# Kernel tuning notes

Measured on AMD Instinct MI355X. Metric: run time of the kernel, lower is better.

Reference implementation:

```python
import jax, jax.numpy as jnp
import numpy as np

C = 256
CQK = C // 8  # 32


def setup_inputs() -> dict:
    key = jax.random.key(0)
    ks = jax.random.split(key, 7)
    x = jax.random.normal(ks[0], (4, C, 64, 64), dtype=jnp.float32)
    s = 1.0 / np.sqrt(C)
    Wq = jax.random.normal(ks[1], (CQK, C), dtype=jnp.float32) * s
    bq = jnp.zeros((CQK,), dtype=jnp.float32)
    Wk = jax.random.normal(ks[2], (CQK, C), dtype=jnp.float32) * s
    bk = jnp.zeros((CQK,), dtype=jnp.float32)
    Wv = jax.random.normal(ks[3], (C, C), dtype=jnp.float32) * s
    bv = jnp.zeros((C,), dtype=jnp.float32)
    return {"x": x, "Wq": Wq, "bq": bq, "Wk": Wk, "bk": bk, "Wv": Wv, "bv": bv}


def reference(x, Wq, bq, Wk, bk, Wv, bv):
    B, Cc, H, W = x.shape
    xf = x.reshape(B, Cc, H * W)  # [B, C, HW]
    # 1x1 convs == per-pixel linear projections over channels
    q = jnp.einsum('oc,bcn->bno', Wq, xf) + bq          # [B, HW, C//8]
    k = jnp.einsum('oc,bcn->bon', Wk, xf) + bk[:, None]  # [B, C//8, HW]
    v = jnp.einsum('oc,bcn->bno', Wv, xf) + bv          # [B, HW, C]
    attn = jax.nn.softmax(jnp.einsum('bnd,bdm->bnm', q, k), axis=-1)  # [B, HW, HW]
    out = jnp.einsum('bnm,bmc->bnc', attn, v)           # [B, HW, C]
    return out.transpose(0, 2, 1).reshape(B, Cc, H, W)
```

## Files before the change

### kernel.cpp

```cpp
#include <hip/hip_runtime.h>
#include <hip/hip_bf16.h>


#define N_PIX 4096
#define DQK   32
#define CCH   256
#define LOG2E 1.44269504088896f

typedef __attribute__((ext_vector_type(8))) _Float16 f16x8;
typedef __attribute__((ext_vector_type(4))) _Float16 f16x4;
typedef __attribute__((ext_vector_type(2))) _Float16 f16x2;
typedef __attribute__((ext_vector_type(8))) short    bf16x8;
typedef __attribute__((ext_vector_type(4))) short    bf16x4;
typedef __attribute__((ext_vector_type(4))) float    f32x4;

__device__ inline void barrier_lds() {
    asm volatile("" ::: "memory");
    __builtin_amdgcn_s_waitcnt(0xc07f);
    __builtin_amdgcn_s_barrier();
    asm volatile("" ::: "memory");
}

__device__ inline short bf16bits(float f) {
    __hip_bfloat16 h = __float2bfloat16(f);
    return *(short*)&h;
}

__device__ inline unsigned cvt_pk_bf16(float lo, float hi) {
    unsigned r;
    asm("v_cvt_pk_bf16_f32 %0, %1, %2" : "=v"(r) : "v"(lo), "v"(hi));
    return r;
}

__global__ __launch_bounds__(256) void wpack_kernel(
    const float* __restrict__ Wq, const float* __restrict__ Wk,
    const float* __restrict__ Wv, _Float16* __restrict__ Wp)
{
    const int tid   = threadIdx.x;
    const int wflat = blockIdx.x * 4 + (tid >> 6);
    const int lane  = tid & 63;
    const int L15   = lane & 15;
    const int quad  = lane >> 4;
    const int mt    = wflat >> 3;
    const int ks    = wflat & 7;
    const int m0    = mt * 16;

    const float* Wsrc; int row; float scale = 1.f;
    if (m0 < 32)      { Wsrc = Wq; row = m0 + L15;      scale = LOG2E; }
    else if (m0 < 64) { Wsrc = Wk; row = m0 - 32 + L15; }
    else              { Wsrc = Wv; row = m0 - 64 + L15; }

    const float* p = Wsrc + (size_t)row * 256 + ks * 32 + quad * 8;
    f16x8 h;
    #pragma unroll
    for (int j = 0; j < 8; ++j) h[j] = (_Float16)(p[j] * scale);
    *(f16x8*)(Wp + ((size_t)wflat * 64 + lane) * 8) = h;
}

__global__ __launch_bounds__(512, 4) void qkv_kernel(
    const float* __restrict__ x, const _Float16* __restrict__ Wp,
    const float* __restrict__ bq, const float* __restrict__ bk,
    const float* __restrict__ bv,
    _Float16* __restrict__ qo, _Float16* __restrict__ ko,
    __hip_bfloat16* __restrict__ vp)
{
    __shared__ alignas(16) unsigned char shraw[256 * 40 * 2];
    _Float16       (*xT)[264] = (_Float16 (*)[264])shraw;
    __hip_bfloat16 (*vst)[40] = (__hip_bfloat16 (*)[40])shraw;

    const int idx = blockIdx.x;
    const int b   = (idx & 7) >> 1;
    const int n0  = (((idx >> 3) << 1) | (idx & 1)) * 32;
    const int tid = threadIdx.x;

    {
        const float* xb = x + (size_t)b * CCH * N_PIX;
        float4 ld[2][2];
        int c2s[2], n4s[2];
        #pragma unroll
        for (int pass = 0; pass < 2; ++pass) {
            const int flat = pass * 512 + tid;
            c2s[pass] = (flat >> 3) * 2;
            n4s[pass] = (flat & 7) * 4;
            ld[pass][0] = *(const float4*)(xb + (size_t)c2s[pass]       * N_PIX + n0 + n4s[pass]);
            ld[pass][1] = *(const float4*)(xb + (size_t)(c2s[pass] + 1) * N_PIX + n0 + n4s[pass]);
        }
        #pragma unroll
        for (int pass = 0; pass < 2; ++pass) {
            const float a[4] = {ld[pass][0].x, ld[pass][0].y, ld[pass][0].z, ld[pass][0].w};
            const float c[4] = {ld[pass][1].x, ld[pass][1].y, ld[pass][1].z, ld[pass][1].w};
            #pragma unroll
            for (int i = 0; i < 4; ++i)
                *(f16x2*)(&xT[n4s[pass] + i][c2s[pass]]) =
                    (f16x2){(_Float16)a[i], (_Float16)c[i]};
        }
    }
    __syncthreads();

    const int lane = tid & 63;
    const int wid  = tid >> 6;
    const int L15  = lane & 15;
    const int quad = lane >> 4;
    const int nf   = wid & 1;
    const int mtg  = wid >> 1;

    const f32x4 fz = {0.f, 0.f, 0.f, 0.f};
    f32x4 acc[5];
    #pragma unroll
    for (int mt = 0; mt < 5; ++mt) acc[mt] = fz;

    const _Float16* wpw = Wp + ((size_t)(mtg * 5) * 8 * 64 + lane) * 8;

    #pragma unroll
    for (int ks = 0; ks < 8; ++ks) {
        const f16x8 bfr = *(const f16x8*)(&xT[nf * 16 + L15][ks * 32 + quad * 8]);
        #pragma unroll
        for (int mt = 0; mt < 5; ++mt) {
            const f16x8 afr = *(const f16x8*)(wpw + (size_t)(mt * 8 + ks) * 512);
            acc[mt] = __builtin_amdgcn_mfma_f32_16x16x32_f16(afr, bfr, acc[mt], 0, 0, 0);
        }
    }

    const int np = nf * 16 + L15;
    const int n  = n0 + np;
    #pragma unroll
    for (int mt = 0; mt < 5; ++mt) {
        const int m0 = (mtg * 5 + mt) * 16;
        const f32x4 a = acc[mt];
        if (m0 < 32) {
            const int mr = m0 + quad * 4;
            f16x4 h;
            #pragma unroll
            for (int r = 0; r < 4; ++r) h[r] = (_Float16)(a[r] + bq[mr + r] * LOG2E);
            *(f16x4*)(qo + ((size_t)b * N_PIX + n) * DQK + mr) = h;
        } else if (m0 < 64) {
            const int mr = m0 - 32 + quad * 4;
            f16x4 h;
            #pragma unroll
            for (int r = 0; r < 4; ++r) h[r] = (_Float16)(a[r] + bk[mr + r]);
            *(f16x4*)(ko + ((size_t)b * N_PIX + n) * DQK + mr) = h;
        }
    }

    __syncthreads();

    #pragma unroll
    for (int mt = 0; mt < 5; ++mt) {
        const int m0 = (mtg * 5 + mt) * 16;
        if (m0 >= 64) {
            const int c = m0 - 64 + quad * 4;
            #pragma unroll
            for (int r = 0; r < 4; ++r)
                vst[c + r][np] = __float2bfloat16(acc[mt][r] + bv[c + r]);
        }
    }
    __syncthreads();

    {
        __hip_bfloat16* vpb = vp + (size_t)b * 2048 * 512 + (size_t)((n0 >> 5) * 16) * 512;
        #pragma unroll
        for (int s = 0; s < 2; ++s) {
            const int slot = s * 512 + tid;
            const int cg16 = slot >> 6;
            const int ln   = slot & 63;
            const int qd   = ln >> 4;
            const int l15  = ln & 15;
            const bf16x8 val = *(const bf16x8*)(&vst[cg16 * 16 + l15][qd * 8]);
            *(bf16x8*)(vpb + ((size_t)cg16 * 64 + ln) * 8) = val;
        }
    }
}


#define ATTN_BODY(J, KR, VR, PSRD, DO_S)                                          \
  {                                                                               \
    const bool dos_ = (DO_S);                                                     \
    f32x4 s_ = fz;                                                                \
    if (dos_) s_ = __builtin_amdgcn_mfma_f32_16x16x32_f16(KR, aq, fz, 0, 0, 0);   \
                        \
    {                                                                             \
      const _Float16* kt_ = kb + (size_t)(((J) + 3) & 63) * (64 * DQK);           \
      KR = *(const f16x8*)(kt_ + koff);                                           \
    }                                                                             \
                                                          \
    _Pragma("unroll")                                                             \
    for (int qq_ = 0; qq_ < 2; ++qq_) {                                           \
      _Pragma("unroll")                                                           \
      for (int kk_ = 0; kk_ < 2; ++kk_) {                                         \
        const bf16x8 ap_ = *(const bf16x8*)(                                      \
            &Ps[PSRD][qq_ * 16 + L15][(kk_ * 32 + quad * 8) ^ sw8]);              \
        oacc[qq_][0] = __builtin_amdgcn_mfma_f32_16x16x32_bf16(                   \
            ap_, VR[kk_][0], oacc[qq_][0], 0, 0, 0);                              \
        oacc[qq_][1] = __builtin_amdgcn_mfma_f32_16x16x32_bf16(                   \
            ap_, VR[kk_][1], oacc[qq_][1], 0, 0, 0);                              \
      }                                                                           \
    }                                                                             \
                                                     \
    {                                                                             \
      const __hip_bfloat16* vt_ = vb + (size_t)(((J) + 2) & 63) * (2 * 16 * 512); \
      _Pragma("unroll")                                                           \
      for (int kk_ = 0; kk_ < 2; ++kk_)                                           \
        _Pragma("unroll")                                                         \
        for (int cf_ = 0; cf_ < 2; ++cf_)                                         \
          VR[kk_][cf_] = *(const bf16x8*)(vt_ + voff0 + kk_ * 8192 + cf_ * 512);  \
    }                                                                             \
                                          \
    if (dos_) {                                                                   \
      const float p0_ = exp2f(s_[0]), p1_ = exp2f(s_[1]);                         \
      const float p2_ = exp2f(s_[2]), p3_ = exp2f(s_[3]);                         \
      psum += (p0_ + p1_) + (p2_ + p3_);                                          \
      uint2 pk_;                                                                  \
      pk_.x = cvt_pk_bf16(p0_, p1_);                                              \
      pk_.y = cvt_pk_bf16(p2_, p3_);                                              \
      *(uint2*)(&Ps[(PSRD) ^ 1][qt * 16 + L15][(kt * 16 + quad * 4) ^ sw8]) = pk_;\
    }                                                                             \
    barrier_lds();                                                                \
  }

__global__ __launch_bounds__(512, 4) void attn_kernel(
    const _Float16* __restrict__ qg,
    const _Float16* __restrict__ kg,
    const __hip_bfloat16* __restrict__ vp,
    float* __restrict__ out)
{
    __shared__ alignas(16) __hip_bfloat16 Ps[2][32][72];
    __shared__ float lsum[2][4][16];

    const int idx  = blockIdx.x;
    const int b    = (idx & 7) >> 1;
    const int n0   = (((idx >> 3) << 1) | (idx & 1)) * 32;
    const int tid  = threadIdx.x;
    const int wid  = tid >> 6;
    const int lane = tid & 63;
    const int L15  = lane & 15;
    const int quad = lane >> 4;
    const int qt   = wid & 1;
    const int kt   = wid >> 1;
    const int cg   = wid;
    const int c0   = cg * 32;
    const int sw8  = ((L15 >> 3) & 1) << 3;

    const f32x4 fz = {0.f, 0.f, 0.f, 0.f};

    const f16x8 aq = *(const f16x8*)(qg + ((size_t)b * N_PIX + n0 + qt * 16 + L15) * DQK + quad * 8);

    f32x4 oacc[2][2];
    #pragma unroll
    for (int qq = 0; qq < 2; ++qq)
        #pragma unroll
        for (int cf = 0; cf < 2; ++cf) oacc[qq][cf] = fz;
    float psum = 0.f;

    const _Float16* kb = kg + (size_t)b * N_PIX * DQK;
    const int koff  = (kt * 16 + L15) * DQK + quad * 8;
    const __hip_bfloat16* vb = vp + (size_t)b * 2048 * 512;
    const int voff0 = lane * 8 + cg * 2 * 512;

    f16x8 kA = *(const f16x8*)(kb + (size_t)1 * 64 * DQK + koff);
    f16x8 kB = *(const f16x8*)(kb + (size_t)2 * 64 * DQK + koff);
    bf16x8 vA[2][2], vB[2][2];
    #pragma unroll
    for (int kk = 0; kk < 2; ++kk)
        #pragma unroll
        for (int cf = 0; cf < 2; ++cf) {
            vA[kk][cf] = *(const bf16x8*)(vb +                 voff0 + kk * 8192 + cf * 512);
            vB[kk][cf] = *(const bf16x8*)(vb + (size_t)16384 + voff0 + kk * 8192 + cf * 512);
        }
    {
        const f16x8 k0f = *(const f16x8*)(kb + koff);
        const f32x4 s = __builtin_amdgcn_mfma_f32_16x16x32_f16(k0f, aq, fz, 0, 0, 0);
        const float p0 = exp2f(s[0]), p1 = exp2f(s[1]);
        const float p2 = exp2f(s[2]), p3 = exp2f(s[3]);
        psum += (p0 + p1) + (p2 + p3);
        uint2 pk;
        pk.x = cvt_pk_bf16(p0, p1);
        pk.y = cvt_pk_bf16(p2, p3);
        *(uint2*)(&Ps[0][qt * 16 + L15][(kt * 16 + quad * 4) ^ sw8]) = pk;
    }
    barrier_lds();

    for (int it = 0; it < 64; it += 2) {
        ATTN_BODY(it,     kA, vA, 0, true);
        ATTN_BODY(it + 1, kB, vB, 1, it < 62);
    }

    psum += __shfl_xor(psum, 16, 64);
    psum += __shfl_xor(psum, 32, 64);
    if (quad == 0) lsum[qt][kt][L15] = psum;
    __syncthreads();

    float* ob = out + (size_t)b * CCH * N_PIX;
    #pragma unroll
    for (int qq = 0; qq < 2; ++qq) {
        float inv_l[4];
        #pragma unroll
        for (int r = 0; r < 4; ++r) {
            const int q = quad * 4 + r;
            inv_l[r] = 1.f / (lsum[qq][0][q] + lsum[qq][1][q] +
                              lsum[qq][2][q] + lsum[qq][3][q]);
        }
        #pragma unroll
        for (int cf = 0; cf < 2; ++cf) {
            const int c = c0 + cf * 16 + L15;
            f32x4 o;
            #pragma unroll
            for (int r = 0; r < 4; ++r) o[r] = oacc[qq][cf][r] * inv_l[r];
            *(f32x4*)(ob + (size_t)c * N_PIX + n0 + qq * 16 + quad * 4) = o;
        }
    }
}

extern "C" void kernel_launch(void* const* d_in, const int* in_sizes, int n_in,
                              void* d_out, int out_size, void* d_ws, size_t ws_size,
                              hipStream_t stream) {
    (void)in_sizes; (void)n_in; (void)out_size; (void)ws_size;
    const float* x  = (const float*)d_in[0];
    const float* Wq = (const float*)d_in[1];
    const float* bq = (const float*)d_in[2];
    const float* Wk = (const float*)d_in[3];
    const float* bk = (const float*)d_in[4];
    const float* Wv = (const float*)d_in[5];
    const float* bv = (const float*)d_in[6];

    _Float16* qb = (_Float16*)d_ws;
    _Float16* kb = qb + (size_t)4 * N_PIX * DQK;
    __hip_bfloat16* vpk = (__hip_bfloat16*)(kb + (size_t)4 * N_PIX * DQK);
    _Float16* wp = (_Float16*)(vpk + (size_t)4 * 2048 * 512);
    float* outp = (float*)d_out;

    wpack_kernel<<<40, 256, 0, stream>>>(Wq, Wk, Wv, wp);
    qkv_kernel<<<512, 512, 0, stream>>>(x, wp, bq, bk, bv, qb, kb, vpk);
    attn_kernel<<<512, 512, 0, stream>>>(qb, kb, vpk, outp);
}
```

Before: 147.8 us.

## Warp-specialize attention into separate score and PV wavefronts with 64-query tiles

Restructures the attention kernel into 1024-thread blocks where 8 wavefronts compute QK scores, exp2 and bf16 P tiles, while 8 other wavefronts consume P from LDS and do the PV MFMAs. Each block now covers 64 queries instead of 32, halving the number of blocks and doubling reuse of each V tile loaded. The P tile in LDS is relaid out as pre-packed MFMA fragments to avoid the swizzle. The two roles hand off through double-buffered LDS with a barrier per step. The design relies on score and PV work overlapping across waves, at the cost of a larger block, fewer blocks (256) and idle lanes in whichever role is lighter.

```diff
diff --git a/kernel.cpp b/kernel.cpp
--- a/kernel.cpp
+++ b/kernel.cpp
@@ -19,11 +19,6 @@
     __builtin_amdgcn_s_waitcnt(0xc07f);
     __builtin_amdgcn_s_barrier();
     asm volatile("" ::: "memory");
-}
-
-__device__ inline short bf16bits(float f) {
-    __hip_bfloat16 h = __float2bfloat16(f);
-    return *(short*)&h;
 }
 
 __device__ inline unsigned cvt_pk_bf16(float lo, float hi) {
@@ -172,140 +167,157 @@
 }
 
 
-#define ATTN_BODY(J, KR, VR, PSRD, DO_S)                                          \
+#define PV_BODY(J, VR)                                                            \
   {                                                                               \
-    const bool dos_ = (DO_S);                                                     \
-    f32x4 s_ = fz;                                                                \
-    if (dos_) s_ = __builtin_amdgcn_mfma_f32_16x16x32_f16(KR, aq, fz, 0, 0, 0);   \
-                        \
-    {                                                                             \
-      const _Float16* kt_ = kb + (size_t)(((J) + 3) & 63) * (64 * DQK);           \
-      KR = *(const f16x8*)(kt_ + koff);                                           \
-    }                                                                             \
-                                                          \
+    const int buf_ = (J) & 1;                                                     \
     _Pragma("unroll")                                                             \
-    for (int qq_ = 0; qq_ < 2; ++qq_) {                                           \
+    for (int qq_ = 0; qq_ < 4; ++qq_) {                                           \
       _Pragma("unroll")                                                           \
       for (int kk_ = 0; kk_ < 2; ++kk_) {                                         \
-        const bf16x8 ap_ = *(const bf16x8*)(                                      \
-            &Ps[PSRD][qq_ * 16 + L15][(kk_ * 32 + quad * 8) ^ sw8]);              \
+        const bf16x8 ap_ = *(const bf16x8*)(&Ps[buf_][qq_ * 2 + kk_][quad][L15][0]); \
         oacc[qq_][0] = __builtin_amdgcn_mfma_f32_16x16x32_bf16(                   \
             ap_, VR[kk_][0], oacc[qq_][0], 0, 0, 0);                              \
         oacc[qq_][1] = __builtin_amdgcn_mfma_f32_16x16x32_bf16(                   \
             ap_, VR[kk_][1], oacc[qq_][1], 0, 0, 0);                              \
       }                                                                           \
     }                                                                             \
-                                                     \
-    {                                                                             \
-      const __hip_bfloat16* vt_ = vb + (size_t)(((J) + 2) & 63) * (2 * 16 * 512); \
+    const __hip_bfloat16* vt_ = vb + (size_t)(((J) + 2) & 63) * 16384;            \
+    _Pragma("unroll")                                                             \
+    for (int kk_ = 0; kk_ < 2; ++kk_)                                             \
       _Pragma("unroll")                                                           \
-      for (int kk_ = 0; kk_ < 2; ++kk_)                                           \
-        _Pragma("unroll")                                                         \
-        for (int cf_ = 0; cf_ < 2; ++cf_)                                         \
-          VR[kk_][cf_] = *(const bf16x8*)(vt_ + voff0 + kk_ * 8192 + cf_ * 512);  \
+      for (int cf_ = 0; cf_ < 2; ++cf_)                                           \
+        VR[kk_][cf_] = *(const bf16x8*)(vt_ + voff0 + kk_ * 8192 + cf_ * 512);    \
+  }
+
+#define S_BODY(J, KR0, KR1, DO_S)                                                 \
+  {                                                                               \
+    if (DO_S) {                                                                   \
+      const int bufw_ = ((J) & 1) ^ 1;                                            \
+      const f32x4 s0_ = __builtin_amdgcn_mfma_f32_16x16x32_f16(KR0, aq, fz, 0, 0, 0); \
+      const f32x4 s1_ = __builtin_amdgcn_mfma_f32_16x16x32_f16(KR1, aq, fz, 0, 0, 0); \
+      const _Float16* kp_ = kbp + (size_t)(((J) + 3) & 63) * (64 * DQK);          \
+      KR0 = *(const f16x8*)(kp_ + koff0);                                         \
+      KR1 = *(const f16x8*)(kp_ + koff1);                                         \
+      const float a0_ = exp2f(s0_[0]), a1_ = exp2f(s0_[1]);                       \
+      const float a2_ = exp2f(s0_[2]), a3_ = exp2f(s0_[3]);                       \
+      psum0 += (a0_ + a1_) + (a2_ + a3_);                                         \
+      uint2 w0_; w0_.x = cvt_pk_bf16(a0_, a1_); w0_.y = cvt_pk_bf16(a2_, a3_);    \
+      *(uint2*)(&Ps[bufw_][grp][quad >> 1][L15][(quad & 1) * 4]) = w0_;           \
+      const float b0_ = exp2f(s1_[0]), b1_ = exp2f(s1_[1]);                       \
+      const float b2_ = exp2f(s1_[2]), b3_ = exp2f(s1_[3]);                       \
+      psum1 += (b0_ + b1_) + (b2_ + b3_);                                         \
+      uint2 w1_; w1_.x = cvt_pk_bf16(b0_, b1_); w1_.y = cvt_pk_bf16(b2_, b3_);    \
+      *(uint2*)(&Ps[bufw_][grp][2 + (quad >> 1)][L15][(quad & 1) * 4]) = w1_;     \
     }                                                                             \
-                                          \
-    if (dos_) {                                                                   \
-      const float p0_ = exp2f(s_[0]), p1_ = exp2f(s_[1]);                         \
-      const float p2_ = exp2f(s_[2]), p3_ = exp2f(s_[3]);                         \
-      psum += (p0_ + p1_) + (p2_ + p3_);                                          \
-      uint2 pk_;                                                                  \
-      pk_.x = cvt_pk_bf16(p0_, p1_);                                              \
-      pk_.y = cvt_pk_bf16(p2_, p3_);                                              \
-      *(uint2*)(&Ps[(PSRD) ^ 1][qt * 16 + L15][(kt * 16 + quad * 4) ^ sw8]) = pk_;\
-    }                                                                             \
-    barrier_lds();                                                                \
   }
 
-__global__ __launch_bounds__(512, 4) void attn_kernel(
+__global__ __launch_bounds__(1024, 4) void attn_kernel(
     const _Float16* __restrict__ qg,
     const _Float16* __restrict__ kg,
     const __hip_bfloat16* __restrict__ vp,
     float* __restrict__ out)
 {
-    __shared__ alignas(16) __hip_bfloat16 Ps[2][32][72];
-    __shared__ float lsum[2][4][16];
+    __shared__ __hip_bfloat16 Ps[2][8][4][16][8];
+    __shared__ float lsum[4][4][16];
 
     const int idx  = blockIdx.x;
     const int b    = (idx & 7) >> 1;
-    const int n0   = (((idx >> 3) << 1) | (idx & 1)) * 32;
+    const int n0   = (((idx >> 3) << 1) | (idx & 1)) * 64;
     const int tid  = threadIdx.x;
     const int wid  = tid >> 6;
     const int lane = tid & 63;
     const int L15  = lane & 15;
     const int quad = lane >> 4;
-    const int qt   = wid & 1;
-    const int kt   = wid >> 1;
-    const int cg   = wid;
-    const int c0   = cg * 32;
-    const int sw8  = ((L15 >> 3) & 1) << 3;
+    const bool is_pv = (wid < 8);
 
     const f32x4 fz = {0.f, 0.f, 0.f, 0.f};
 
-    const f16x8 aq = *(const f16x8*)(qg + ((size_t)b * N_PIX + n0 + qt * 16 + L15) * DQK + quad * 8);
-
-    f32x4 oacc[2][2];
-    #pragma unroll
-    for (int qq = 0; qq < 2; ++qq)
-        #pragma unroll
-        for (int cf = 0; cf < 2; ++cf) oacc[qq][cf] = fz;
-    float psum = 0.f;
-
-    const _Float16* kb = kg + (size_t)b * N_PIX * DQK;
-    const int koff  = (kt * 16 + L15) * DQK + quad * 8;
+    const int cg = wid & 7;
     const __hip_bfloat16* vb = vp + (size_t)b * 2048 * 512;
     const int voff0 = lane * 8 + cg * 2 * 512;
-
-    f16x8 kA = *(const f16x8*)(kb + (size_t)1 * 64 * DQK + koff);
-    f16x8 kB = *(const f16x8*)(kb + (size_t)2 * 64 * DQK + koff);
+    f32x4 oacc[4][2];
+    #pragma unroll
+    for (int qq = 0; qq < 4; ++qq) { oacc[qq][0] = fz; oacc[qq][1] = fz; }
     bf16x8 vA[2][2], vB[2][2];
-    #pragma unroll
-    for (int kk = 0; kk < 2; ++kk)
-        #pragma unroll
-        for (int cf = 0; cf < 2; ++cf) {
-            vA[kk][cf] = *(const bf16x8*)(vb +                 voff0 + kk * 8192 + cf * 512);
-            vB[kk][cf] = *(const bf16x8*)(vb + (size_t)16384 + voff0 + kk * 8192 + cf * 512);
-        }
-    {
-        const f16x8 k0f = *(const f16x8*)(kb + koff);
-        const f32x4 s = __builtin_amdgcn_mfma_f32_16x16x32_f16(k0f, aq, fz, 0, 0, 0);
-        const float p0 = exp2f(s[0]), p1 = exp2f(s[1]);
-        const float p2 = exp2f(s[2]), p3 = exp2f(s[3]);
-        psum += (p0 + p1) + (p2 + p3);
-        uint2 pk;
-        pk.x = cvt_pk_bf16(p0, p1);
-        pk.y = cvt_pk_bf16(p2, p3);
-        *(uint2*)(&Ps[0][qt * 16 + L15][(kt * 16 + quad * 4) ^ sw8]) = pk;
+
+    const int sqt  = (wid & 7) >> 1;
+    const int kt0  = (wid & 1) * 2;
+    const int grp  = wid & 7;
+    const _Float16* kbp = kg + (size_t)b * N_PIX * DQK;
+    const int koff0 = ((kt0 + 0) * 16 + L15) * DQK + quad * 8;
+    const int koff1 = ((kt0 + 1) * 16 + L15) * DQK + quad * 8;
+    f16x8 aq{}, kA0{}, kA1{}, kB0{}, kB1{};
+    float psum0 = 0.f, psum1 = 0.f;
+
+    if (is_pv) {
+        #pragma unroll
+        for (int kk = 0; kk < 2; ++kk)
+            #pragma unroll
+            for (int cf = 0; cf < 2; ++cf) {
+                vA[kk][cf] = *(const bf16x8*)(vb +         voff0 + kk * 8192 + cf * 512);
+                vB[kk][cf] = *(const bf16x8*)(vb + 16384 + voff0 + kk * 8192 + cf * 512);
+            }
+    } else {
+        aq = *(const f16x8*)(qg + ((size_t)b * N_PIX + n0 + sqt * 16 + L15) * DQK + quad * 8);
+        const f16x8 k00 = *(const f16x8*)(kbp + koff0);
+        const f16x8 k01 = *(const f16x8*)(kbp + koff1);
+        kA0 = *(const f16x8*)(kbp + (size_t)1 * 64 * DQK + koff0);
+        kA1 = *(const f16x8*)(kbp + (size_t)1 * 64 * DQK + koff1);
+        kB0 = *(const f16x8*)(kbp + (size_t)2 * 64 * DQK + koff0);
+        kB1 = *(const f16x8*)(kbp + (size_t)2 * 64 * DQK + koff1);
+        const f32x4 s0 = __builtin_amdgcn_mfma_f32_16x16x32_f16(k00, aq, fz, 0, 0, 0);
+        const f32x4 s1 = __builtin_amdgcn_mfma_f32_16x16x32_f16(k01, aq, fz, 0, 0, 0);
+        const float a0 = exp2f(s0[0]), a1 = exp2f(s0[1]);
+        const float a2 = exp2f(s0[2]), a3 = exp2f(s0[3]);
+        psum0 += (a0 + a1) + (a2 + a3);
+        uint2 w0; w0.x = cvt_pk_bf16(a0, a1); w0.y = cvt_pk_bf16(a2, a3);
+        *(uint2*)(&Ps[0][grp][quad >> 1][L15][(quad & 1) * 4]) = w0;
+        const float b0 = exp2f(s1[0]), b1 = exp2f(s1[1]);
+        const float b2 = exp2f(s1[2]), b3 = exp2f(s1[3]);
+        psum1 += (b0 + b1) + (b2 + b3);
+        uint2 w1; w1.x = cvt_pk_bf16(b0, b1); w1.y = cvt_pk_bf16(b2, b3);
+        *(uint2*)(&Ps[0][grp][2 + (quad >> 1)][L15][(quad & 1) * 4]) = w1;
     }
     barrier_lds();
 
     for (int it = 0; it < 64; it += 2) {
-        ATTN_BODY(it,     kA, vA, 0, true);
-        ATTN_BODY(it + 1, kB, vB, 1, it < 62);
-    }
-
-    psum += __shfl_xor(psum, 16, 64);
-    psum += __shfl_xor(psum, 32, 64);
-    if (quad == 0) lsum[qt][kt][L15] = psum;
+        if (is_pv) { PV_BODY(it, vA) } else { S_BODY(it, kA0, kA1, true) }
+        barrier_lds();
+        if (is_pv) { PV_BODY(it + 1, vB) } else { S_BODY(it + 1, kB0, kB1, it < 62) }
+        barrier_lds();
+    }
+
+    if (!is_pv) {
+        psum0 += __shfl_xor(psum0, 16, 64);
+        psum0 += __shfl_xor(psum0, 32, 64);
+        psum1 += __shfl_xor(psum1, 16, 64);
+        psum1 += __shfl_xor(psum1, 32, 64);
+        if (quad == 0) {
+            lsum[sqt][kt0 + 0][L15] = psum0;
+            lsum[sqt][kt0 + 1][L15] = psum1;
+        }
+    }
     __syncthreads();
 
-    float* ob = out + (size_t)b * CCH * N_PIX;
-    #pragma unroll
-    for (int qq = 0; qq < 2; ++qq) {
-        float inv_l[4];
-        #pragma unroll
-        for (int r = 0; r < 4; ++r) {
-            const int q = quad * 4 + r;
-            inv_l[r] = 1.f / (lsum[qq][0][q] + lsum[qq][1][q] +
-                              lsum[qq][2][q] + lsum[qq][3][q]);
-        }
-        #pragma unroll
-        for (int cf = 0; cf < 2; ++cf) {
-            const int c = c0 + cf * 16 + L15;
-            f32x4 o;
-            #pragma unroll
-            for (int r = 0; r < 4; ++r) o[r] = oacc[qq][cf][r] * inv_l[r];
-            *(f32x4*)(ob + (size_t)c * N_PIX + n0 + qq * 16 + quad * 4) = o;
+    if (is_pv) {
+        float* ob = out + (size_t)b * CCH * N_PIX;
+        #pragma unroll
+        for (int qq = 0; qq < 4; ++qq) {
+            float inv_l[4];
+            #pragma unroll
+            for (int r = 0; r < 4; ++r) {
+                const int q = quad * 4 + r;
+                inv_l[r] = 1.f / (lsum[qq][0][q] + lsum[qq][1][q] +
+                                  lsum[qq][2][q] + lsum[qq][3][q]);
+            }
+            #pragma unroll
+            for (int cf = 0; cf < 2; ++cf) {
+                const int c = cg * 32 + cf * 16 + L15;
+                f32x4 o;
+                #pragma unroll
+                for (int r = 0; r < 4; ++r) o[r] = oacc[qq][cf][r] * inv_l[r];
+                *(f32x4*)(ob + (size_t)c * N_PIX + n0 + qq * 16 + quad * 4) = o;
+            }
         }
     }
 }
@@ -330,5 +342,5 @@
 
     wpack_kernel<<<40, 256, 0, stream>>>(Wq, Wk, Wv, wp);
     qkv_kernel<<<512, 512, 0, stream>>>(x, wp, bq, bk, bv, qb, kb, vpk);
-    attn_kernel<<<512, 512, 0, stream>>>(qb, kb, vpk, outp);
-}
+    attn_kernel<<<256, 1024, 0, stream>>>(qb, kb, vpk, outp);
+}
```

Measured after the change: 140.3 us. 1.05x faster.
